# Kernel tuning notes

Hardware: AMD Instinct MI355X
Metric: run time of the kernel (lower is better)

Reference implementation:

```python
import jax, jax.numpy as jnp
import numpy as np

N, E = 50000, 800000
D_IN, D_H, D_OUT = 128, 128, 64


def setup_inputs() -> dict:
    key = jax.random.key(0)
    ks = jax.random.split(key, 12)
    x = jax.random.normal(ks[0], (N, D_IN), dtype=jnp.float32)
    edge_index = jax.random.randint(ks[1], (2, E), 0, N, dtype=jnp.int64)
    s = 0.05
    return {
        "x": x,
        "edge_index": edge_index,
        # SAGEConv layer 0: in -> hidden. lin_l (neighbor path, with bias), lin_r (root, no bias)
        "Wl0": jax.random.normal(ks[2], (D_H, D_IN), dtype=jnp.float32) * s,
        "bl0": jnp.zeros((D_H,), dtype=jnp.float32),
        "Wr0": jax.random.normal(ks[3], (D_H, D_IN), dtype=jnp.float32) * s,
        # layer 1: hidden -> hidden
        "Wl1": jax.random.normal(ks[4], (D_H, D_H), dtype=jnp.float32) * s,
        "bl1": jnp.zeros((D_H,), dtype=jnp.float32),
        "Wr1": jax.random.normal(ks[5], (D_H, D_H), dtype=jnp.float32) * s,
        # layer 2: hidden -> out
        "Wl2": jax.random.normal(ks[6], (D_OUT, D_H), dtype=jnp.float32) * s,
        "bl2": jnp.zeros((D_OUT,), dtype=jnp.float32),
        "Wr2": jax.random.normal(ks[7], (D_OUT, D_H), dtype=jnp.float32) * s,
    }


def reference(x, edge_index, Wl0, bl0, Wr0, Wl1, bl1, Wr1, Wl2, bl2, Wr2):
    n = x.shape[0]
    src, dst = edge_index[0], edge_index[1]
    # in-degree of each target node (mean aggregation denominator)
    deg = jax.ops.segment_sum(jnp.ones_like(dst, dtype=x.dtype), dst, num_segments=n)
    inv_deg = (1.0 / jnp.maximum(deg, 1.0))[:, None]  # [N,1]; zero-degree -> sum is 0 anyway

    def sage_conv(h, Wl, bl, Wr):
        # mean-aggregate neighbor features: gather h[src], scatter-add to dst
        agg = jax.ops.segment_sum(h[src], dst, num_segments=n) * inv_deg  # [N, d]
        return agg @ Wl.T + bl + h @ Wr.T

    h = jax.nn.relu(sage_conv(x, Wl0, bl0, Wr0))
    # dropout p=0 in eval mode (training=False, force_dropout=False) -> no-op
    h = jax.nn.relu(sage_conv(h, Wl1, bl1, Wr1))
    return sage_conv(h, Wl2, bl2, Wr2)
```

## Files before the change

kernel.cpp:

```cpp
#include <hip/hip_runtime.h>


#define D_H 128
#define NBUCKET 196
#define EPB 8192
#define NBLK 98

typedef _Float16 half8  __attribute__((ext_vector_type(8)));
typedef _Float16 half4v __attribute__((ext_vector_type(4)));
typedef float    floatx4 __attribute__((ext_vector_type(4)));

__global__ __launch_bounds__(256) void hist_wconv_kernel(
        const int* __restrict__ dst, int* __restrict__ histo, int E,
        const float* __restrict__ w0, const float* __restrict__ w1,
        const float* __restrict__ w2, const float* __restrict__ w3,
        const float* __restrict__ w4, const float* __restrict__ w5,
        _Float16* __restrict__ o0, _Float16* __restrict__ o1,
        _Float16* __restrict__ o2, _Float16* __restrict__ o3,
        _Float16* __restrict__ o4, _Float16* __restrict__ o5) {
    if (blockIdx.x < NBLK) {
        __shared__ int h[NBUCKET];
        for (int i = threadIdx.x; i < NBUCKET; i += 256) h[i] = 0;
        __syncthreads();
        int base = blockIdx.x * EPB;
        int end = min(base + EPB, E);
        for (int i = base + threadIdx.x; i < end; i += 256)
            atomicAdd(&h[dst[i] >> 8], 1);
        __syncthreads();
        for (int i = threadIdx.x; i < NBUCKET; i += 256)
            histo[blockIdx.x * NBUCKET + i] = h[i];
        return;
    }
    int k = (blockIdx.x - NBLK) * 256 + threadIdx.x;
    const float* in; _Float16* out; int j;
    if      (k <  4096) { in = w0; out = o0; j = k; }
    else if (k <  8192) { in = w1; out = o1; j = k - 4096; }
    else if (k < 12288) { in = w2; out = o2; j = k - 8192; }
    else if (k < 16384) { in = w3; out = o3; j = k - 12288; }
    else if (k < 18432) { in = w4; out = o4; j = k - 16384; }
    else if (k < 20480) { in = w5; out = o5; j = k - 18432; }
    else return;
    float4 v = ((const float4*)in)[j];
    half4v o = { (_Float16)v.x, (_Float16)v.y, (_Float16)v.z, (_Float16)v.w };
    ((half4v*)out)[j] = o;
}

template<bool F32A>
__device__ __forceinline__ void dual_tile(
        const float* __restrict__ Af, const _Float16* __restrict__ Ah,
        const _Float16* __restrict__ Wl, const _Float16* __restrict__ Wr,
        const float* __restrict__ bias,
        _Float16* __restrict__ T, _Float16* __restrict__ R,
        int N, int g) {
    const int ntile = (N + 63) >> 6;
    if (g >= 2 * ntile) return;
    const bool rpass = g >= ntile;
    const _Float16* __restrict__ W = rpass ? Wr : Wl;
    _Float16* __restrict__ O = rpass ? R : T;
    const int tile = rpass ? g - ntile : g;
    const int lt   = threadIdx.x & 127;
    const int wave = lt >> 6;
    const int lane = lt & 63;
    const int r16  = lane & 15;
    const int quad = lane >> 4;
    const int base = tile * 64 + wave * 32;
    const int koff = quad * 8;
    const int row0 = min(base + r16,      N - 1);
    const int row1 = min(base + 16 + r16, N - 1);

    floatx4 acc[2][8];
    #pragma unroll
    for (int s = 0; s < 2; ++s)
        #pragma unroll
        for (int j = 0; j < 8; ++j)
            acc[s][j] = (floatx4){0.f, 0.f, 0.f, 0.f};

    #pragma unroll
    for (int k0 = 0; k0 < 128; k0 += 32) {
        half8 a0, a1;
        if (F32A) {
            float4 p0 = *(const float4*)&Af[(size_t)row0 * 128 + k0 + koff];
            float4 p1 = *(const float4*)&Af[(size_t)row0 * 128 + k0 + koff + 4];
            float4 q0 = *(const float4*)&Af[(size_t)row1 * 128 + k0 + koff];
            float4 q1 = *(const float4*)&Af[(size_t)row1 * 128 + k0 + koff + 4];
            a0 = (half8){ (_Float16)p0.x, (_Float16)p0.y, (_Float16)p0.z, (_Float16)p0.w,
                          (_Float16)p1.x, (_Float16)p1.y, (_Float16)p1.z, (_Float16)p1.w };
            a1 = (half8){ (_Float16)q0.x, (_Float16)q0.y, (_Float16)q0.z, (_Float16)q0.w,
                          (_Float16)q1.x, (_Float16)q1.y, (_Float16)q1.z, (_Float16)q1.w };
        } else {
            a0 = *(const half8*)&Ah[(size_t)row0 * 128 + k0 + koff];
            a1 = *(const half8*)&Ah[(size_t)row1 * 128 + k0 + koff];
        }
        #pragma unroll
        for (int j = 0; j < 8; ++j) {
            half8 b = *(const half8*)&W[(size_t)(j * 16 + r16) * 128 + k0 + koff];
            acc[0][j] = __builtin_amdgcn_mfma_f32_16x16x32_f16(a0, b, acc[0][j], 0, 0, 0);
            acc[1][j] = __builtin_amdgcn_mfma_f32_16x16x32_f16(a1, b, acc[1][j], 0, 0, 0);
        }
    }

    #pragma unroll
    for (int s = 0; s < 2; ++s)
        #pragma unroll
        for (int i = 0; i < 4; ++i) {
            int r = base + s * 16 + quad * 4 + i;
            if (r >= N) continue;
            #pragma unroll
            for (int j = 0; j < 8; ++j) {
                int c = j * 16 + r16;
                float v = acc[s][j][i];
                if (rpass) v += bias[c];
                O[(size_t)r * 128 + c] = (_Float16)v;
            }
        }
}

__global__ __launch_bounds__(256) void scan_gemm_kernel(
        const int* __restrict__ histo, int* __restrict__ offs,
        int* __restrict__ boff, int* __restrict__ row_ptr, int n,
        const float* __restrict__ x, const _Float16* __restrict__ Wl,
        const _Float16* __restrict__ Wr, const float* __restrict__ bias,
        _Float16* __restrict__ T, _Float16* __restrict__ R, int gofs) {
    if (blockIdx.x == 0) {
        __shared__ int s[256];
        int t = threadIdx.x;
        int sum = 0;
        if (t < NBUCKET) {
            for (int b = 0; b < NBLK; ++b) {
                offs[b * NBUCKET + t] = sum;
                sum += histo[b * NBUCKET + t];
            }
        }
        s[t] = (t < NBUCKET) ? sum : 0;
        int tot = s[t];
        __syncthreads();
        for (int off = 1; off < 256; off <<= 1) {
            int tmp = (t >= off) ? s[t - off] : 0;
            __syncthreads();
            s[t] += tmp;
            __syncthreads();
        }
        int base = s[t] - tot;
        if (t < NBUCKET) boff[t] = base;
        if (t == 255) { boff[NBUCKET] = s[255]; row_ptr[n] = s[255]; }
        __syncthreads();
        if (t < NBUCKET)
            for (int b = 0; b < NBLK; ++b)
                offs[b * NBUCKET + t] += base;
        return;
    }
    int g = (blockIdx.x - 1) * 2 + (threadIdx.x >> 7) + gofs;
    dual_tile<true>(x, nullptr, Wl, Wr, bias, T, R, n, g);
}

__global__ __launch_bounds__(256) void scatter_gemm_kernel(
        const int* __restrict__ src, const int* __restrict__ dst,
        const int* __restrict__ offs, unsigned int* __restrict__ bedge, int E,
        const float* __restrict__ x, const _Float16* __restrict__ Wl,
        const _Float16* __restrict__ Wr, const float* __restrict__ bias,
        _Float16* __restrict__ T, _Float16* __restrict__ R, int N, int gofs) {
    if (blockIdx.x < NBLK) {
        __shared__ int lcur[NBUCKET];
        for (int i = threadIdx.x; i < NBUCKET; i += 256)
            lcur[i] = offs[blockIdx.x * NBUCKET + i];
        __syncthreads();
        int base = blockIdx.x * EPB;
        int end = min(base + EPB, E);
        for (int i = base + threadIdx.x; i < end; i += 256) {
            int d = dst[i];
            int pos = atomicAdd(&lcur[d >> 8], 1);
            bedge[pos] = ((unsigned int)(d & 255) << 16) | (unsigned int)src[i];
        }
        return;
    }
    int g = (blockIdx.x - NBLK) * 2 + (threadIdx.x >> 7) + gofs;
    dual_tile<true>(x, nullptr, Wl, Wr, bias, T, R, N, g);
}

__global__ __launch_bounds__(256) void bucket_gemm_kernel(
        const unsigned int* __restrict__ bedge, const int* __restrict__ boff,
        int* __restrict__ row_ptr, float* __restrict__ inv_deg,
        int* __restrict__ col, int n,
        const float* __restrict__ x, const _Float16* __restrict__ Wl,
        const _Float16* __restrict__ Wr, const float* __restrict__ bias,
        _Float16* __restrict__ T, _Float16* __restrict__ R, int gofs) {
    if (blockIdx.x < NBUCKET) {
        __shared__ int sdeg[256];
        __shared__ int sscan[256];
        __shared__ int lcur[256];
        const int b = blockIdx.x;
        const int t = threadIdx.x;
        const int base = boff[b];
        const int bend = boff[b + 1];
        sdeg[t] = 0;
        __syncthreads();
        for (int i = base + t; i < bend; i += 256)
            atomicAdd(&sdeg[bedge[i] >> 16], 1);
        __syncthreads();
        int d = sdeg[t];
        sscan[t] = d;
        __syncthreads();
        for (int off = 1; off < 256; off <<= 1) {
            int tmp = (t >= off) ? sscan[t - off] : 0;
            __syncthreads();
            sscan[t] += tmp;
            __syncthreads();
        }
        int excl = sscan[t] - d;
        int node = b * 256 + t;
        if (node < n) {
            row_ptr[node] = base + excl;
            inv_deg[node] = 1.0f / (float)max(d, 1);
        }
        lcur[t] = excl;
        __syncthreads();
        for (int i = base + t; i < bend; i += 256) {
            unsigned int v = bedge[i];
            int pos = atomicAdd(&lcur[v >> 16], 1);
            col[base + pos] = (int)(v & 0xffffu);
        }
        return;
    }
    int g = (blockIdx.x - NBUCKET) * 2 + (threadIdx.x >> 7) + gofs;
    dual_tile<true>(x, nullptr, Wl, Wr, bias, T, R, n, g);
}

__global__ __launch_bounds__(256) void dual_fp16_kernel(
        const _Float16* __restrict__ A, const _Float16* __restrict__ Wl,
        const _Float16* __restrict__ Wr, const float* __restrict__ bias,
        _Float16* __restrict__ T, _Float16* __restrict__ R, int N) {
    int g = blockIdx.x * 2 + (threadIdx.x >> 7);
    dual_tile<false>(nullptr, A, Wl, Wr, bias, T, R, N, g);
}

__global__ __launch_bounds__(128, 8) void agg_relu_kernel(
        const _Float16* __restrict__ T, const _Float16* __restrict__ R,
        const int* __restrict__ row_ptr, const int* __restrict__ col,
        const float* __restrict__ inv_deg, _Float16* __restrict__ h, int n) {
    int wave = threadIdx.x >> 6;
    int lane = threadIdx.x & 63;
    int node = blockIdx.x * 2 + wave;
    if (node >= n) return;
    int beg = row_ptr[node];
    int end = row_ptr[node + 1];
    const int quarter = lane >> 4;
    const int off = (lane & 15) << 3;
    float a0f = 0.f, a1f = 0.f, a2f = 0.f, a3f = 0.f;
    float a4f = 0.f, a5f = 0.f, a6f = 0.f, a7f = 0.f;
    for (int base = beg; base < end; base += 64) {
        int m = end - base;
        if (m > 64) m = 64;
        int myc = (lane < m) ? col[base + lane] : 0;
        int t = 0;
        for (; t + 4 <= (m >> 2); t += 4) {
            int u0 = __shfl(myc, ((t + 0) << 2) + quarter);
            int u1 = __shfl(myc, ((t + 1) << 2) + quarter);
            int u2 = __shfl(myc, ((t + 2) << 2) + quarter);
            int u3 = __shfl(myc, ((t + 3) << 2) + quarter);
            half8 v0 = *(const half8*)&T[(size_t)u0 * D_H + off];
            half8 v1 = *(const half8*)&T[(size_t)u1 * D_H + off];
            half8 v2 = *(const half8*)&T[(size_t)u2 * D_H + off];
            half8 v3 = *(const half8*)&T[(size_t)u3 * D_H + off];
            a0f += (float)v0[0] + (float)v1[0] + (float)v2[0] + (float)v3[0];
            a1f += (float)v0[1] + (float)v1[1] + (float)v2[1] + (float)v3[1];
            a2f += (float)v0[2] + (float)v1[2] + (float)v2[2] + (float)v3[2];
            a3f += (float)v0[3] + (float)v1[3] + (float)v2[3] + (float)v3[3];
            a4f += (float)v0[4] + (float)v1[4] + (float)v2[4] + (float)v3[4];
            a5f += (float)v0[5] + (float)v1[5] + (float)v2[5] + (float)v3[5];
            a6f += (float)v0[6] + (float)v1[6] + (float)v2[6] + (float)v3[6];
            a7f += (float)v0[7] + (float)v1[7] + (float)v2[7] + (float)v3[7];
        }
        int smax = (m + 3) >> 2;
        for (; t < smax; ++t) {
            int j = (t << 2) + quarter;
            int u = __shfl(myc, j);
            if (j < m) {
                half8 v = *(const half8*)&T[(size_t)u * D_H + off];
                a0f += (float)v[0]; a1f += (float)v[1];
                a2f += (float)v[2]; a3f += (float)v[3];
                a4f += (float)v[4]; a5f += (float)v[5];
                a6f += (float)v[6]; a7f += (float)v[7];
            }
        }
    }
    a0f += __shfl(a0f, lane + 16); a1f += __shfl(a1f, lane + 16);
    a2f += __shfl(a2f, lane + 16); a3f += __shfl(a3f, lane + 16);
    a4f += __shfl(a4f, lane + 16); a5f += __shfl(a5f, lane + 16);
    a6f += __shfl(a6f, lane + 16); a7f += __shfl(a7f, lane + 16);
    a0f += __shfl(a0f, lane + 32); a1f += __shfl(a1f, lane + 32);
    a2f += __shfl(a2f, lane + 32); a3f += __shfl(a3f, lane + 32);
    a4f += __shfl(a4f, lane + 32); a5f += __shfl(a5f, lane + 32);
    a6f += __shfl(a6f, lane + 32); a7f += __shfl(a7f, lane + 32);
    if (quarter == 0) {
        float s = inv_deg[node];
        half8 r = *(const half8*)&R[(size_t)node * D_H + off];
        half8 o = { (_Float16)fmaxf((float)r[0] + a0f * s, 0.f),
                    (_Float16)fmaxf((float)r[1] + a1f * s, 0.f),
                    (_Float16)fmaxf((float)r[2] + a2f * s, 0.f),
                    (_Float16)fmaxf((float)r[3] + a3f * s, 0.f),
                    (_Float16)fmaxf((float)r[4] + a4f * s, 0.f),
                    (_Float16)fmaxf((float)r[5] + a5f * s, 0.f),
                    (_Float16)fmaxf((float)r[6] + a6f * s, 0.f),
                    (_Float16)fmaxf((float)r[7] + a7f * s, 0.f) };
        *(half8*)&h[(size_t)node * D_H + off] = o;
    }
}

__global__ __launch_bounds__(128, 8) void aggregate_add64_kernel(
        const _Float16* __restrict__ T,
        const _Float16* __restrict__ Rh,
        const int* __restrict__ row_ptr,
        const int* __restrict__ col,
        const float* __restrict__ inv_deg,
        float* __restrict__ out, int n) {
    int wave = threadIdx.x >> 6;
    int lane = threadIdx.x & 63;
    int node = blockIdx.x * 2 + wave;
    if (node >= n) return;
    int beg = row_ptr[node];
    int end = row_ptr[node + 1];
    const int quarter = lane >> 4;
    const int off = (lane & 15) << 2;
    float a0f = 0.f, a1f = 0.f, a2f = 0.f, a3f = 0.f;
    for (int base = beg; base < end; base += 64) {
        int m = end - base;
        if (m > 64) m = 64;
        int myc = (lane < m) ? col[base + lane] : 0;
        int t = 0;
        for (; t + 4 <= (m >> 2); t += 4) {
            int u0 = __shfl(myc, ((t + 0) << 2) + quarter);
            int u1 = __shfl(myc, ((t + 1) << 2) + quarter);
            int u2 = __shfl(myc, ((t + 2) << 2) + quarter);
            int u3 = __shfl(myc, ((t + 3) << 2) + quarter);
            half4v v0 = *(const half4v*)&T[(size_t)u0 * 64 + off];
            half4v v1 = *(const half4v*)&T[(size_t)u1 * 64 + off];
            half4v v2 = *(const half4v*)&T[(size_t)u2 * 64 + off];
            half4v v3 = *(const half4v*)&T[(size_t)u3 * 64 + off];
            a0f += (float)v0[0] + (float)v1[0] + (float)v2[0] + (float)v3[0];
            a1f += (float)v0[1] + (float)v1[1] + (float)v2[1] + (float)v3[1];
            a2f += (float)v0[2] + (float)v1[2] + (float)v2[2] + (float)v3[2];
            a3f += (float)v0[3] + (float)v1[3] + (float)v2[3] + (float)v3[3];
        }
        int smax = (m + 3) >> 2;
        for (; t < smax; ++t) {
            int j = (t << 2) + quarter;
            int u = __shfl(myc, j);
            if (j < m) {
                half4v v = *(const half4v*)&T[(size_t)u * 64 + off];
                a0f += (float)v[0]; a1f += (float)v[1];
                a2f += (float)v[2]; a3f += (float)v[3];
            }
        }
    }
    a0f += __shfl(a0f, lane + 16); a1f += __shfl(a1f, lane + 16);
    a2f += __shfl(a2f, lane + 16); a3f += __shfl(a3f, lane + 16);
    a0f += __shfl(a0f, lane + 32); a1f += __shfl(a1f, lane + 32);
    a2f += __shfl(a2f, lane + 32); a3f += __shfl(a3f, lane + 32);
    if (quarter == 0) {
        float s = inv_deg[node];
        half4v r = *(const half4v*)&Rh[(size_t)node * 64 + off];
        float4 o;
        o.x = (float)r[0] + a0f * s;
        o.y = (float)r[1] + a1f * s;
        o.z = (float)r[2] + a2f * s;
        o.w = (float)r[3] + a3f * s;
        *(float4*)&out[(size_t)node * 64 + off] = o;
    }
}

__global__ __launch_bounds__(128) void gemm_dual_kernel(
        const _Float16* __restrict__ B, const _Float16* __restrict__ Wl,
        const _Float16* __restrict__ Wr, const float* __restrict__ bias,
        _Float16* __restrict__ T, _Float16* __restrict__ Rh, int N) {
    const int wave = threadIdx.x >> 6;
    const int lane = threadIdx.x & 63;
    const int r16 = lane & 15;
    const int quad = lane >> 4;
    const int base = blockIdx.x * 64 + wave * 32;
    const int koff = quad * 8;

    floatx4 accT[2][4], accR[2][4];
    #pragma unroll
    for (int s = 0; s < 2; ++s)
        #pragma unroll
        for (int j = 0; j < 4; ++j) {
            accT[s][j] = (floatx4){0.f, 0.f, 0.f, 0.f};
            accR[s][j] = (floatx4){0.f, 0.f, 0.f, 0.f};
        }

    #pragma unroll
    for (int k0 = 0; k0 < 128; k0 += 32) {
        half8 a0 = *(const half8*)&B[(size_t)(base + r16) * 128 + k0 + koff];
        half8 a1 = *(const half8*)&B[(size_t)(base + 16 + r16) * 128 + k0 + koff];
        #pragma unroll
        for (int j = 0; j < 4; ++j) {
            half8 bl = *(const half8*)&Wl[(size_t)(j * 16 + r16) * 128 + k0 + koff];
            half8 br = *(const half8*)&Wr[(size_t)(j * 16 + r16) * 128 + k0 + koff];
            accT[0][j] = __builtin_amdgcn_mfma_f32_16x16x32_f16(a0, bl, accT[0][j], 0, 0, 0);
            accT[1][j] = __builtin_amdgcn_mfma_f32_16x16x32_f16(a1, bl, accT[1][j], 0, 0, 0);
            accR[0][j] = __builtin_amdgcn_mfma_f32_16x16x32_f16(a0, br, accR[0][j], 0, 0, 0);
            accR[1][j] = __builtin_amdgcn_mfma_f32_16x16x32_f16(a1, br, accR[1][j], 0, 0, 0);
        }
    }

    #pragma unroll
    for (int s = 0; s < 2; ++s) {
        #pragma unroll
        for (int i = 0; i < 4; ++i) {
            int r = base + s * 16 + quad * 4 + i;
            if (r >= N) continue;
            #pragma unroll
            for (int j = 0; j < 4; ++j) {
                int c = j * 16 + r16;
                T[(size_t)r * 64 + c]  = (_Float16)accT[s][j][i];
                Rh[(size_t)r * 64 + c] = (_Float16)(accR[s][j][i] + bias[c]);
            }
        }
    }
}

extern "C" void kernel_launch(void* const* d_in, const int* in_sizes, int n_in,
                              void* d_out, int out_size, void* d_ws, size_t ws_size,
                              hipStream_t stream) {
    const float* x   = (const float*)d_in[0];
    const int*   edge = (const int*)d_in[1];
    const float* Wl0 = (const float*)d_in[2];
    const float* bl0 = (const float*)d_in[3];
    const float* Wr0 = (const float*)d_in[4];
    const float* Wl1 = (const float*)d_in[5];
    const float* bl1 = (const float*)d_in[6];
    const float* Wr1 = (const float*)d_in[7];
    const float* Wl2 = (const float*)d_in[8];
    const float* bl2 = (const float*)d_in[9];
    const float* Wr2 = (const float*)d_in[10];
    float* out = (float*)d_out;

    const int N = in_sizes[0] / D_H;
    const int E = in_sizes[1] / 2;
    const int* src = edge;
    const int* dst = edge + E;

    const int gx = (N + 63) / 64;
    const int Np = gx * 64;
    const size_t HBYTES = (size_t)Np * D_H * 2;

    char* w = (char*)d_ws;
    _Float16* Tb = (_Float16*)w;  w += HBYTES;
    _Float16* Rb = (_Float16*)w;  w += HBYTES;
    _Float16* Hb = (_Float16*)w;  w += HBYTES;
    _Float16* Wl0h = (_Float16*)w;  w += (size_t)128 * 128 * 2;
    _Float16* Wr0h = (_Float16*)w;  w += (size_t)128 * 128 * 2;
    _Float16* Wl1h = (_Float16*)w;  w += (size_t)128 * 128 * 2;
    _Float16* Wr1h = (_Float16*)w;  w += (size_t)128 * 128 * 2;
    _Float16* Wl2h = (_Float16*)w;  w += (size_t)64 * 128 * 2;
    _Float16* Wr2h = (_Float16*)w;  w += (size_t)64 * 128 * 2;
    int* row_ptr = (int*)w;      w += (size_t)(N + 16) * 4;
    float* inv_deg = (float*)w;  w += (size_t)N * 4;
    int* col     = (int*)w;      w += (size_t)E * 4;
    int* histo   = (int*)w;      w += (size_t)NBLK * NBUCKET * 4;
    int* offs    = (int*)w;      w += (size_t)NBLK * NBUCKET * 4;
    int* boff    = (int*)w;      w += (size_t)(NBUCKET + 1) * 4;
    unsigned int* bedge = (unsigned int*)w;  w += (size_t)E * 4;

    hist_wconv_kernel<<<NBLK + 80, 256, 0, stream>>>(
        dst, histo, E,
        Wl0, Wr0, Wl1, Wr1, Wl2, Wr2,
        Wl0h, Wr0h, Wl1h, Wr1h, Wl2h, Wr2h);

    const int C0 = 260, C1 = 260, C2 = gx - C0 - C1;
    scan_gemm_kernel<<<1 + C0, 256, 0, stream>>>(
        histo, offs, boff, row_ptr, N,
        x, Wl0h, Wr0h, bl0, Tb, Rb, 0);
    scatter_gemm_kernel<<<NBLK + C1, 256, 0, stream>>>(
        src, dst, offs, bedge, E,
        x, Wl0h, Wr0h, bl0, Tb, Rb, N, 2 * C0);
    bucket_gemm_kernel<<<NBUCKET + C2, 256, 0, stream>>>(
        bedge, boff, row_ptr, inv_deg, col, N,
        x, Wl0h, Wr0h, bl0, Tb, Rb, 2 * (C0 + C1));

    const int agg_grid = (N + 1) / 2;

    agg_relu_kernel<<<agg_grid, 128, 0, stream>>>(Tb, Rb, row_ptr, col, inv_deg, Hb, N);

    dual_fp16_kernel<<<gx, 256, 0, stream>>>(Hb, Wl1h, Wr1h, bl1, Tb, Rb, N);
    agg_relu_kernel<<<agg_grid, 128, 0, stream>>>(Tb, Rb, row_ptr, col, inv_deg, Hb, N);

    gemm_dual_kernel<<<gx, 128, 0, stream>>>(Hb, Wl2h, Wr2h, bl2, Tb, Rb, N);
    aggregate_add64_kernel<<<agg_grid, 128, 0, stream>>>(Tb, Rb, row_ptr, col,
                                                         inv_deg, out, N);
}
```

Measured before the change: 298.9 us.

## Aggregate before transform in layer 1 with a single concatenated-K MFMA GEMM

Layer 1 used to transform first and aggregate after: a dual GEMM wrote T and R, then agg_relu gathered T. Now the hidden features are mean-aggregated first, and one GEMM then consumes both the aggregated and root inputs, adding bias and ReLU in its epilogue. This removes the separate R buffer write and the fused agg+add pass. The fp16 dual-tile template collapses to an f32-only helper, and the layer-2 buffers are aliased into Hb. The gather still moves 128-wide rows, so traffic is about the same, but the kernel split and intermediate writes change.

Result: faster. 288.6 us (-3.4%).

```diff
diff --git a/kernel.cpp b/kernel.cpp
--- a/kernel.cpp
+++ b/kernel.cpp
@@ -45,9 +45,8 @@
     ((half4v*)out)[j] = o;
 }
 
-template<bool F32A>
-__device__ __forceinline__ void dual_tile(
-        const float* __restrict__ Af, const _Float16* __restrict__ Ah,
+__device__ __forceinline__ void dual_tile_f32(
+        const float* __restrict__ Af,
         const _Float16* __restrict__ Wl, const _Float16* __restrict__ Wr,
         const float* __restrict__ bias,
         _Float16* __restrict__ T, _Float16* __restrict__ R,
@@ -77,20 +76,14 @@
 
     #pragma unroll
     for (int k0 = 0; k0 < 128; k0 += 32) {
-        half8 a0, a1;
-        if (F32A) {
-            float4 p0 = *(const float4*)&Af[(size_t)row0 * 128 + k0 + koff];
-            float4 p1 = *(const float4*)&Af[(size_t)row0 * 128 + k0 + koff + 4];
-            float4 q0 = *(const float4*)&Af[(size_t)row1 * 128 + k0 + koff];
-            float4 q1 = *(const float4*)&Af[(size_t)row1 * 128 + k0 + koff + 4];
-            a0 = (half8){ (_Float16)p0.x, (_Float16)p0.y, (_Float16)p0.z, (_Float16)p0.w,
-                          (_Float16)p1.x, (_Float16)p1.y, (_Float16)p1.z, (_Float16)p1.w };
-            a1 = (half8){ (_Float16)q0.x, (_Float16)q0.y, (_Float16)q0.z, (_Float16)q0.w,
-                          (_Float16)q1.x, (_Float16)q1.y, (_Float16)q1.z, (_Float16)q1.w };
-        } else {
-            a0 = *(const half8*)&Ah[(size_t)row0 * 128 + k0 + koff];
-            a1 = *(const half8*)&Ah[(size_t)row1 * 128 + k0 + koff];
-        }
+        float4 p0 = *(const float4*)&Af[(size_t)row0 * 128 + k0 + koff];
+        float4 p1 = *(const float4*)&Af[(size_t)row0 * 128 + k0 + koff + 4];
+        float4 q0 = *(const float4*)&Af[(size_t)row1 * 128 + k0 + koff];
+        float4 q1 = *(const float4*)&Af[(size_t)row1 * 128 + k0 + koff + 4];
+        half8 a0 = (half8){ (_Float16)p0.x, (_Float16)p0.y, (_Float16)p0.z, (_Float16)p0.w,
+                            (_Float16)p1.x, (_Float16)p1.y, (_Float16)p1.z, (_Float16)p1.w };
+        half8 a1 = (half8){ (_Float16)q0.x, (_Float16)q0.y, (_Float16)q0.z, (_Float16)q0.w,
+                            (_Float16)q1.x, (_Float16)q1.y, (_Float16)q1.z, (_Float16)q1.w };
         #pragma unroll
         for (int j = 0; j < 8; ++j) {
             half8 b = *(const half8*)&W[(size_t)(j * 16 + r16) * 128 + k0 + koff];
@@ -150,7 +143,7 @@
         return;
     }
     int g = (blockIdx.x - 1) * 2 + (threadIdx.x >> 7) + gofs;
-    dual_tile<true>(x, nullptr, Wl, Wr, bias, T, R, n, g);
+    dual_tile_f32(x, Wl, Wr, bias, T, R, n, g);
 }
 
 __global__ __launch_bounds__(256) void scatter_gemm_kernel(
@@ -174,7 +167,7 @@
         return;
     }
     int g = (blockIdx.x - NBLK) * 2 + (threadIdx.x >> 7) + gofs;
-    dual_tile<true>(x, nullptr, Wl, Wr, bias, T, R, N, g);
+    dual_tile_f32(x, Wl, Wr, bias, T, R, N, g);
 }
 
 __global__ __launch_bounds__(256) void bucket_gemm_kernel(
@@ -222,15 +215,7 @@
         return;
     }
     int g = (blockIdx.x - NBUCKET) * 2 + (threadIdx.x >> 7) + gofs;
-    dual_tile<true>(x, nullptr, Wl, Wr, bias, T, R, n, g);
-}
-
-__global__ __launch_bounds__(256) void dual_fp16_kernel(
-        const _Float16* __restrict__ A, const _Float16* __restrict__ Wl,
-        const _Float16* __restrict__ Wr, const float* __restrict__ bias,
-        _Float16* __restrict__ T, _Float16* __restrict__ R, int N) {
-    int g = blockIdx.x * 2 + (threadIdx.x >> 7);
-    dual_tile<false>(nullptr, A, Wl, Wr, bias, T, R, N, g);
+    dual_tile_f32(x, Wl, Wr, bias, T, R, n, g);
 }
 
 __global__ __launch_bounds__(128, 8) void agg_relu_kernel(
@@ -306,6 +291,184 @@
     }
 }
 
+__global__ __launch_bounds__(128, 8) void aggregate_kernel(const _Float16* __restrict__ h,
+                                                           const int* __restrict__ row_ptr,
+                                                           const int* __restrict__ col,
+                                                           const float* __restrict__ inv_deg,
+                                                           _Float16* __restrict__ agg, int n) {
+    int wave = threadIdx.x >> 6;
+    int lane = threadIdx.x & 63;
+    int node = blockIdx.x * 2 + wave;
+    if (node >= n) return;
+    int beg = row_ptr[node];
+    int end = row_ptr[node + 1];
+    const int quarter = lane >> 4;
+    const int off = (lane & 15) << 3;
+    float a0f = 0.f, a1f = 0.f, a2f = 0.f, a3f = 0.f;
+    float a4f = 0.f, a5f = 0.f, a6f = 0.f, a7f = 0.f;
+    for (int base = beg; base < end; base += 64) {
+        int m = end - base;
+        if (m > 64) m = 64;
+        int myc = (lane < m) ? col[base + lane] : 0;
+        int t = 0;
+        for (; t + 4 <= (m >> 2); t += 4) {
+            int u0 = __shfl(myc, ((t + 0) << 2) + quarter);
+            int u1 = __shfl(myc, ((t + 1) << 2) + quarter);
+            int u2 = __shfl(myc, ((t + 2) << 2) + quarter);
+            int u3 = __shfl(myc, ((t + 3) << 2) + quarter);
+            half8 v0 = *(const half8*)&h[(size_t)u0 * D_H + off];
+            half8 v1 = *(const half8*)&h[(size_t)u1 * D_H + off];
+            half8 v2 = *(const half8*)&h[(size_t)u2 * D_H + off];
+            half8 v3 = *(const half8*)&h[(size_t)u3 * D_H + off];
+            a0f += (float)v0[0] + (float)v1[0] + (float)v2[0] + (float)v3[0];
+            a1f += (float)v0[1] + (float)v1[1] + (float)v2[1] + (float)v3[1];
+            a2f += (float)v0[2] + (float)v1[2] + (float)v2[2] + (float)v3[2];
+            a3f += (float)v0[3] + (float)v1[3] + (float)v2[3] + (float)v3[3];
+            a4f += (float)v0[4] + (float)v1[4] + (float)v2[4] + (float)v3[4];
+            a5f += (float)v0[5] + (float)v1[5] + (float)v2[5] + (float)v3[5];
+            a6f += (float)v0[6] + (float)v1[6] + (float)v2[6] + (float)v3[6];
+            a7f += (float)v0[7] + (float)v1[7] + (float)v2[7] + (float)v3[7];
+        }
+        int smax = (m + 3) >> 2;
+        for (; t < smax; ++t) {
+            int j = (t << 2) + quarter;
+            int u = __shfl(myc, j);
+            if (j < m) {
+                half8 v = *(const half8*)&h[(size_t)u * D_H + off];
+                a0f += (float)v[0]; a1f += (float)v[1];
+                a2f += (float)v[2]; a3f += (float)v[3];
+                a4f += (float)v[4]; a5f += (float)v[5];
+                a6f += (float)v[6]; a7f += (float)v[7];
+            }
+        }
+    }
+    a0f += __shfl(a0f, lane + 16); a1f += __shfl(a1f, lane + 16);
+    a2f += __shfl(a2f, lane + 16); a3f += __shfl(a3f, lane + 16);
+    a4f += __shfl(a4f, lane + 16); a5f += __shfl(a5f, lane + 16);
+    a6f += __shfl(a6f, lane + 16); a7f += __shfl(a7f, lane + 16);
+    a0f += __shfl(a0f, lane + 32); a1f += __shfl(a1f, lane + 32);
+    a2f += __shfl(a2f, lane + 32); a3f += __shfl(a3f, lane + 32);
+    a4f += __shfl(a4f, lane + 32); a5f += __shfl(a5f, lane + 32);
+    a6f += __shfl(a6f, lane + 32); a7f += __shfl(a7f, lane + 32);
+    if (quarter == 0) {
+        float s = inv_deg[node];
+        half8 o = { (_Float16)(a0f * s), (_Float16)(a1f * s),
+                    (_Float16)(a2f * s), (_Float16)(a3f * s),
+                    (_Float16)(a4f * s), (_Float16)(a5f * s),
+                    (_Float16)(a6f * s), (_Float16)(a7f * s) };
+        *(half8*)&agg[(size_t)node * D_H + off] = o;
+    }
+}
+
+template<int NT, bool RELU_HALF_OUT>
+__global__ __launch_bounds__(128) void gemm_mfma_kernel(
+        const _Float16* __restrict__ Xa, const _Float16* __restrict__ Xh,
+        const _Float16* __restrict__ Wa, const _Float16* __restrict__ Wh,
+        const float* __restrict__ bias,
+        _Float16* __restrict__ out_h, float* __restrict__ out_f, int N) {
+    const int wave = threadIdx.x >> 6;
+    const int lane = threadIdx.x & 63;
+    const int r16 = lane & 15;
+    const int quad = lane >> 4;
+    const int base = blockIdx.x * 64 + wave * 32;
+    const int koff = quad * 8;
+
+    floatx4 acc[2][NT];
+    #pragma unroll
+    for (int s = 0; s < 2; ++s)
+        #pragma unroll
+        for (int j = 0; j < NT; ++j)
+            acc[s][j] = (floatx4){0.f, 0.f, 0.f, 0.f};
+
+    #pragma unroll
+    for (int hsel = 0; hsel < 2; ++hsel) {
+        const _Float16* __restrict__ X = hsel ? Xh : Xa;
+        const _Float16* __restrict__ W = hsel ? Wh : Wa;
+        #pragma unroll
+        for (int k0 = 0; k0 < 128; k0 += 32) {
+            half8 a0 = *(const half8*)&X[(size_t)(base + r16) * 128 + k0 + koff];
+            half8 a1 = *(const half8*)&X[(size_t)(base + 16 + r16) * 128 + k0 + koff];
+            #pragma unroll
+            for (int j = 0; j < NT; ++j) {
+                half8 b = *(const half8*)&W[(size_t)(j * 16 + r16) * 128 + k0 + koff];
+                acc[0][j] = __builtin_amdgcn_mfma_f32_16x16x32_f16(a0, b, acc[0][j], 0, 0, 0);
+                acc[1][j] = __builtin_amdgcn_mfma_f32_16x16x32_f16(a1, b, acc[1][j], 0, 0, 0);
+            }
+        }
+    }
+
+    #pragma unroll
+    for (int s = 0; s < 2; ++s) {
+        #pragma unroll
+        for (int i = 0; i < 4; ++i) {
+            int r = base + s * 16 + quad * 4 + i;
+            if (r >= N) continue;
+            #pragma unroll
+            for (int j = 0; j < NT; ++j) {
+                int c = j * 16 + r16;
+                float v = acc[s][j][i] + bias[c];
+                if (RELU_HALF_OUT) {
+                    v = fmaxf(v, 0.f);
+                    out_h[(size_t)r * (NT * 16) + c] = (_Float16)v;
+                } else {
+                    out_f[(size_t)r * (NT * 16) + c] = v;
+                }
+            }
+        }
+    }
+}
+
+__global__ __launch_bounds__(128) void gemm_dual_kernel(
+        const _Float16* __restrict__ B, const _Float16* __restrict__ Wl,
+        const _Float16* __restrict__ Wr, const float* __restrict__ bias,
+        _Float16* __restrict__ T, _Float16* __restrict__ Rh, int N) {
+    const int wave = threadIdx.x >> 6;
+    const int lane = threadIdx.x & 63;
+    const int r16 = lane & 15;
+    const int quad = lane >> 4;
+    const int base = blockIdx.x * 64 + wave * 32;
+    const int koff = quad * 8;
+
+    floatx4 accT[2][4], accR[2][4];
+    #pragma unroll
+    for (int s = 0; s < 2; ++s)
+        #pragma unroll
+        for (int j = 0; j < 4; ++j) {
+            accT[s][j] = (floatx4){0.f, 0.f, 0.f, 0.f};
+            accR[s][j] = (floatx4){0.f, 0.f, 0.f, 0.f};
+        }
+
+    #pragma unroll
+    for (int k0 = 0; k0 < 128; k0 += 32) {
+        half8 a0 = *(const half8*)&B[(size_t)(base + r16) * 128 + k0 + koff];
+        half8 a1 = *(const half8*)&B[(size_t)(base + 16 + r16) * 128 + k0 + koff];
+        #pragma unroll
+        for (int j = 0; j < 4; ++j) {
+            half8 bl = *(const half8*)&Wl[(size_t)(j * 16 + r16) * 128 + k0 + koff];
+            half8 br = *(const half8*)&Wr[(size_t)(j * 16 + r16) * 128 + k0 + koff];
+            accT[0][j] = __builtin_amdgcn_mfma_f32_16x16x32_f16(a0, bl, accT[0][j], 0, 0, 0);
+            accT[1][j] = __builtin_amdgcn_mfma_f32_16x16x32_f16(a1, bl, accT[1][j], 0, 0, 0);
+            accR[0][j] = __builtin_amdgcn_mfma_f32_16x16x32_f16(a0, br, accR[0][j], 0, 0, 0);
+            accR[1][j] = __builtin_amdgcn_mfma_f32_16x16x32_f16(a1, br, accR[1][j], 0, 0, 0);
+        }
+    }
+
+    #pragma unroll
+    for (int s = 0; s < 2; ++s) {
+        #pragma unroll
+        for (int i = 0; i < 4; ++i) {
+            int r = base + s * 16 + quad * 4 + i;
+            if (r >= N) continue;
+            #pragma unroll
+            for (int j = 0; j < 4; ++j) {
+                int c = j * 16 + r16;
+                T[(size_t)r * 64 + c]  = (_Float16)accT[s][j][i];
+                Rh[(size_t)r * 64 + c] = (_Float16)(accR[s][j][i] + bias[c]);
+            }
+        }
+    }
+}
+
 __global__ __launch_bounds__(128, 8) void aggregate_add64_kernel(
         const _Float16* __restrict__ T,
         const _Float16* __restrict__ Rh,
@@ -368,57 +531,6 @@
     }
 }
 
-__global__ __launch_bounds__(128) void gemm_dual_kernel(
-        const _Float16* __restrict__ B, const _Float16* __restrict__ Wl,
-        const _Float16* __restrict__ Wr, const float* __restrict__ bias,
-        _Float16* __restrict__ T, _Float16* __restrict__ Rh, int N) {
-    const int wave = threadIdx.x >> 6;
-    const int lane = threadIdx.x & 63;
-    const int r16 = lane & 15;
-    const int quad = lane >> 4;
-    const int base = blockIdx.x * 64 + wave * 32;
-    const int koff = quad * 8;
-
-    floatx4 accT[2][4], accR[2][4];
-    #pragma unroll
-    for (int s = 0; s < 2; ++s)
-        #pragma unroll
-        for (int j = 0; j < 4; ++j) {
-            accT[s][j] = (floatx4){0.f, 0.f, 0.f, 0.f};
-            accR[s][j] = (floatx4){0.f, 0.f, 0.f, 0.f};
-        }
-
-    #pragma unroll
-    for (int k0 = 0; k0 < 128; k0 += 32) {
-        half8 a0 = *(const half8*)&B[(size_t)(base + r16) * 128 + k0 + koff];
-        half8 a1 = *(const half8*)&B[(size_t)(base + 16 + r16) * 128 + k0 + koff];
-        #pragma unroll
-        for (int j = 0; j < 4; ++j) {
-            half8 bl = *(const half8*)&Wl[(size_t)(j * 16 + r16) * 128 + k0 + koff];
-            half8 br = *(const half8*)&Wr[(size_t)(j * 16 + r16) * 128 + k0 + koff];
-            accT[0][j] = __builtin_amdgcn_mfma_f32_16x16x32_f16(a0, bl, accT[0][j], 0, 0, 0);
-            accT[1][j] = __builtin_amdgcn_mfma_f32_16x16x32_f16(a1, bl, accT[1][j], 0, 0, 0);
-            accR[0][j] = __builtin_amdgcn_mfma_f32_16x16x32_f16(a0, br, accR[0][j], 0, 0, 0);
-            accR[1][j] = __builtin_amdgcn_mfma_f32_16x16x32_f16(a1, br, accR[1][j], 0, 0, 0);
-        }
-    }
-
-    #pragma unroll
-    for (int s = 0; s < 2; ++s) {
-        #pragma unroll
-        for (int i = 0; i < 4; ++i) {
-            int r = base + s * 16 + quad * 4 + i;
-            if (r >= N) continue;
-            #pragma unroll
-            for (int j = 0; j < 4; ++j) {
-                int c = j * 16 + r16;
-                T[(size_t)r * 64 + c]  = (_Float16)accT[s][j][i];
-                Rh[(size_t)r * 64 + c] = (_Float16)(accR[s][j][i] + bias[c]);
-            }
-        }
-    }
-}
-
 extern "C" void kernel_launch(void* const* d_in, const int* in_sizes, int n_in,
                               void* d_out, int out_size, void* d_ws, size_t ws_size,
                               hipStream_t stream) {
@@ -462,6 +574,9 @@
     int* boff    = (int*)w;      w += (size_t)(NBUCKET + 1) * 4;
     unsigned int* bedge = (unsigned int*)w;  w += (size_t)E * 4;
 
+    _Float16* T2  = (_Float16*)Hb;
+    _Float16* Rh2 = (_Float16*)((char*)Hb + HBYTES / 2);
+
     hist_wconv_kernel<<<NBLK + 80, 256, 0, stream>>>(
         dst, histo, E,
         Wl0, Wr0, Wl1, Wr1, Wl2, Wr2,
@@ -482,10 +597,10 @@
 
     agg_relu_kernel<<<agg_grid, 128, 0, stream>>>(Tb, Rb, row_ptr, col, inv_deg, Hb, N);
 
-    dual_fp16_kernel<<<gx, 256, 0, stream>>>(Hb, Wl1h, Wr1h, bl1, Tb, Rb, N);
-    agg_relu_kernel<<<agg_grid, 128, 0, stream>>>(Tb, Rb, row_ptr, col, inv_deg, Hb, N);
-
-    gemm_dual_kernel<<<gx, 128, 0, stream>>>(Hb, Wl2h, Wr2h, bl2, Tb, Rb, N);
-    aggregate_add64_kernel<<<agg_grid, 128, 0, stream>>>(Tb, Rb, row_ptr, col,
+    aggregate_kernel<<<agg_grid, 128, 0, stream>>>(Hb, row_ptr, col, inv_deg, Rb, N);
+    gemm_mfma_kernel<8, true><<<gx, 128, 0, stream>>>(Rb, Hb, Wl1h, Wr1h, bl1, Tb, nullptr, N);
+
+    gemm_dual_kernel<<<gx, 128, 0, stream>>>(Tb, Wl2h, Wr2h, bl2, T2, Rh2, N);
+    aggregate_add64_kernel<<<agg_grid, 128, 0, stream>>>(T2, Rh2, row_ptr, col,
                                                          inv_deg, out, N);
 }
```
